# Kernel optimization log

Hardware: AMD Instinct MI355X
Metric: run time of the kernel (lower is better)

The kernel has to match this reference:

```python
import jax, jax.numpy as jnp
import numpy as np

B, T, H, E, D, K = 4, 4096, 2048, 8, 1024, 2

def setup_inputs() -> dict:
    key = jax.random.key(0)
    ks = jax.random.split(key, 7)
    x  = jax.random.normal(ks[0], (B, T, H), dtype=jnp.float32)
    Wr = jax.random.normal(ks[1], (H, E), dtype=jnp.float32) * (1.0 / np.sqrt(H))
    br = jnp.zeros((E,), dtype=jnp.float32)
    We = jax.random.normal(ks[2], (E, H, D), dtype=jnp.float32) * (1.0 / np.sqrt(H))
    be = jnp.zeros((E, D), dtype=jnp.float32)
    Wc = jax.random.normal(ks[3], (D, H), dtype=jnp.float32) * (1.0 / np.sqrt(D))
    bc = jnp.zeros((H,), dtype=jnp.float32)
    return {"x": x, "Wr": Wr, "br": br, "We": We, "be": be, "Wc": Wc, "bc": bc}

def reference(x, Wr, br, We, be, Wc, bc):
    # Router: [B,T,H] @ [H,E] -> [B,T,E]
    router_logits = jnp.einsum('bth,he->bte', x, Wr) + br
    scores = jax.nn.softmax(router_logits, axis=-1)
    # top-k over experts (sorted descending, like torch.topk)
    topk_scores, topk_idx = jax.lax.top_k(scores, K)  # [B,T,K]
    # Dense all-expert linear: [B,T,E,D]
    expert_outs = jnp.einsum('bth,ehd->bted', x, We) + be
    # Gather the chosen experts per token: [B,T,K,D]
    gather_idx = jnp.broadcast_to(topk_idx[..., None], (B, T, K, D))
    chosen = jnp.take_along_axis(expert_outs, gather_idx, axis=2)
    # Weighted sum over top-k: [B,T,D]
    weighted = jnp.sum(chosen * topk_scores[..., None], axis=2)
    # Combine: [B,T,D] @ [D,H] -> [B,T,H]
    return jnp.einsum('btd,dh->bth', weighted, Wc) + bc
```

## Files before the change

### kernel.cpp

```cpp
#include <hip/hip_runtime.h>
#include <hip/hip_bf16.h>

typedef float f32x4 __attribute__((ext_vector_type(4)));
typedef short bf16x8 __attribute__((ext_vector_type(8)));

#define M_NT 16
#define M_OFF 17
#define M_TBL 32
#define MAX_TILES 264
#define NCHUNK 1024

__device__ __forceinline__ void gload16(const void* g, void* l) {
  __builtin_amdgcn_global_load_lds(
      (const __attribute__((address_space(1))) void*)g,
      (__attribute__((address_space(3))) void*)l, 16, 0, 0);
}

__device__ __forceinline__ float bf2f(unsigned short u) {
  union { unsigned int i; float f; } v; v.i = ((unsigned int)u) << 16; return v.f;
}
__device__ __forceinline__ unsigned short f2bf(float f) {
  __hip_bfloat16 h = __float2bfloat16(f);
  return __builtin_bit_cast(unsigned short, h);
}

#define CBAR() do { asm volatile("" ::: "memory"); __builtin_amdgcn_s_barrier(); asm volatile("" ::: "memory"); } while (0)
#define VMC4() asm volatile("s_waitcnt vmcnt(4)" ::: "memory")
#define VMC0() asm volatile("s_waitcnt vmcnt(0)" ::: "memory")

__global__ __launch_bounds__(256) void prep_kernel(
    const float* __restrict__ x, const float* __restrict__ Wr,
    const float* __restrict__ br, unsigned short* __restrict__ xbf,
    float* __restrict__ scores, int* __restrict__ idx,
    int* __restrict__ blk_hist,
    const float* __restrict__ We, unsigned short* __restrict__ WeT,
    const float* __restrict__ Wc, unsigned short* __restrict__ WcT) {
  __shared__ float tile[32][33];
  __shared__ int cnt[8];
  int blk = blockIdx.x;
  int tid = threadIdx.x;
  if (blk < NCHUNK) {
    int lane = tid & 63, w = tid >> 6;
    if (tid < 8) cnt[tid] = 0;
    __syncthreads();
    int t0 = blk * 16 + w * 4;
    const float* xr = x + (size_t)t0 * 2048;
    unsigned short* xo = xbf + (size_t)t0 * 2048;
    float acc[4][8] = {};
#pragma unroll
    for (int j = 0; j < 8; ++j) {
      int h0 = j * 256 + lane * 4;
      float4 xv[4];
#pragma unroll
      for (int t = 0; t < 4; ++t) xv[t] = *(const float4*)(xr + (size_t)t * 2048 + h0);
#pragma unroll
      for (int t = 0; t < 4; ++t) {
        ushort4 p;
        p.x = f2bf(xv[t].x); p.y = f2bf(xv[t].y);
        p.z = f2bf(xv[t].z); p.w = f2bf(xv[t].w);
        *(ushort4*)(xo + (size_t)t * 2048 + h0) = p;
      }
      const float4* wp = (const float4*)(Wr + (size_t)h0 * 8);
#pragma unroll
      for (int c = 0; c < 4; ++c) {
        float4 w0 = wp[2 * c], w1 = wp[2 * c + 1];
        float xc0 = (c == 0) ? xv[0].x : (c == 1) ? xv[0].y : (c == 2) ? xv[0].z : xv[0].w;
        float xc1 = (c == 0) ? xv[1].x : (c == 1) ? xv[1].y : (c == 2) ? xv[1].z : xv[1].w;
        float xc2 = (c == 0) ? xv[2].x : (c == 1) ? xv[2].y : (c == 2) ? xv[2].z : xv[2].w;
        float xc3 = (c == 0) ? xv[3].x : (c == 1) ? xv[3].y : (c == 2) ? xv[3].z : xv[3].w;
        acc[0][0] += xc0 * w0.x; acc[0][1] += xc0 * w0.y; acc[0][2] += xc0 * w0.z; acc[0][3] += xc0 * w0.w;
        acc[0][4] += xc0 * w1.x; acc[0][5] += xc0 * w1.y; acc[0][6] += xc0 * w1.z; acc[0][7] += xc0 * w1.w;
        acc[1][0] += xc1 * w0.x; acc[1][1] += xc1 * w0.y; acc[1][2] += xc1 * w0.z; acc[1][3] += xc1 * w0.w;
        acc[1][4] += xc1 * w1.x; acc[1][5] += xc1 * w1.y; acc[1][6] += xc1 * w1.z; acc[1][7] += xc1 * w1.w;
        acc[2][0] += xc2 * w0.x; acc[2][1] += xc2 * w0.y; acc[2][2] += xc2 * w0.z; acc[2][3] += xc2 * w0.w;
        acc[2][4] += xc2 * w1.x; acc[2][5] += xc2 * w1.y; acc[2][6] += xc2 * w1.z; acc[2][7] += xc2 * w1.w;
        acc[3][0] += xc3 * w0.x; acc[3][1] += xc3 * w0.y; acc[3][2] += xc3 * w0.z; acc[3][3] += xc3 * w0.w;
        acc[3][4] += xc3 * w1.x; acc[3][5] += xc3 * w1.y; acc[3][6] += xc3 * w1.z; acc[3][7] += xc3 * w1.w;
      }
    }
#pragma unroll
    for (int t = 0; t < 4; ++t)
#pragma unroll
      for (int e = 0; e < 8; ++e)
#pragma unroll
        for (int off = 32; off > 0; off >>= 1)
          acc[t][e] += __shfl_xor(acc[t][e], off);
    if (lane < 4) {
      int t = t0 + lane;
      float l[8];
#pragma unroll
      for (int e = 0; e < 8; ++e) {
        float v = (lane == 0) ? acc[0][e] : (lane == 1) ? acc[1][e]
                : (lane == 2) ? acc[2][e] : acc[3][e];
        l[e] = v + br[e];
      }
      float mx = l[0];
#pragma unroll
      for (int e = 1; e < 8; ++e) mx = fmaxf(mx, l[e]);
      float se = 0.f;
#pragma unroll
      for (int e = 0; e < 8; ++e) se += __expf(l[e] - mx);
      float inv = 1.f / se;
      int e1 = 0; float b1 = l[0];
#pragma unroll
      for (int e = 1; e < 8; ++e) if (l[e] > b1) { b1 = l[e]; e1 = e; }
      int e2 = -1; float b2 = -1e30f;
#pragma unroll
      for (int e = 0; e < 8; ++e) if (e != e1 && l[e] > b2) { b2 = l[e]; e2 = e; }
      idx[2 * t] = e1; idx[2 * t + 1] = e2;
      scores[2 * t] = __expf(b1 - mx) * inv;
      scores[2 * t + 1] = __expf(b2 - mx) * inv;
      atomicAdd(&cnt[e1], 1);
      atomicAdd(&cnt[e2], 1);
    }
    __syncthreads();
    if (tid < 8) blk_hist[blk * 8 + tid] = cnt[tid];
  } else if (blk < NCHUNK + 16384) {
    int i2 = blk - NCHUNK;
    int b = i2 >> 11, rem = i2 & 2047;
    int r0 = (rem >> 5) * 32, c0 = (rem & 31) * 32;
    const float* src = We + (size_t)b * 2048 * 1024;
    unsigned short* dst = WeT + (size_t)b * 2048 * 1024;
    int tx = tid & 31, ty = tid >> 5;
#pragma unroll
    for (int i = 0; i < 32; i += 8)
      tile[ty + i][tx] = src[(size_t)(r0 + ty + i) * 1024 + c0 + tx];
    __syncthreads();
#pragma unroll
    for (int i = 0; i < 32; i += 8)
      dst[(size_t)(c0 + ty + i) * 2048 + r0 + tx] = f2bf(tile[tx][ty + i]);
  } else {
    int i2 = blk - NCHUNK - 16384;
    int r0 = (i2 >> 6) * 32, c0 = (i2 & 63) * 32;
    int tx = tid & 31, ty = tid >> 5;
#pragma unroll
    for (int i = 0; i < 32; i += 8)
      tile[ty + i][tx] = Wc[(size_t)(r0 + ty + i) * 2048 + c0 + tx];
    __syncthreads();
#pragma unroll
    for (int i = 0; i < 32; i += 8)
      WcT[(size_t)(c0 + ty + i) * 1024 + r0 + tx] = f2bf(tile[tx][ty + i]);
  }
}

__global__ __launch_bounds__(512) void scan_kernel(
    const int* __restrict__ blk_hist, int* __restrict__ chunk_base,
    int* __restrict__ meta, int* __restrict__ rowlist) {
  __shared__ int stot[8], soff[8], stbase[8];
  int tid = threadIdx.x, lane = tid & 63, e = tid >> 6;
  int running = 0;
  for (int g = 0; g < NCHUNK / 64; ++g) {
    int c = g * 64 + lane;
    int v = blk_hist[c * 8 + e];
    int orig = v;
#pragma unroll
    for (int off = 1; off < 64; off <<= 1) {
      int n = __shfl_up(v, off);
      if (lane >= off) v += n;
    }
    chunk_base[c * 8 + e] = running + v - orig;
    running += __shfl(v, 63);
  }
  if (lane == 0) stot[e] = running;
  __syncthreads();
  if (tid == 0) {
    int off = 0, nt = 0;
    for (int ee = 0; ee < 8; ++ee) {
      meta[M_OFF + ee] = off; soff[ee] = off;
      int tiles = (stot[ee] + 127) >> 7;
      stbase[ee] = nt;
      nt += tiles;
      off += tiles << 7;
    }
    meta[M_NT] = nt;
  }
  __syncthreads();
  int4* tbl = (int4*)(meta + M_TBL);
  for (int ee = 0; ee < 8; ++ee) {
    int c = stot[ee], tiles = (c + 127) >> 7;
    for (int t = tid; t < tiles; t += 512)
      tbl[stbase[ee] + t] = make_int4(ee, soff[ee] + t * 128, min(128, c - t * 128), 0);
    int end = tiles << 7;
    for (int i = c + tid; i < end; i += 512) rowlist[soff[ee] + i] = 0;
  }
}

__global__ void scatter_kernel(const int* __restrict__ idx,
                               const int* __restrict__ chunk_base,
                               const int* __restrict__ meta,
                               int* __restrict__ rowlist) {
  int c = blockIdx.x, lane = threadIdx.x;
  int entry = c * 32 + lane;
  int e = (lane < 32) ? idx[entry] : -1;
#pragma unroll
  for (int ee = 0; ee < 8; ++ee) {
    unsigned long long m = __ballot(e == ee);
    if (e == ee) {
      int rank = __popcll(m & ((1ull << lane) - 1));
      rowlist[meta[M_OFF + ee] + chunk_base[c * 8 + ee] + rank] = entry;
    }
  }
}


#define RD_FRAGS(BUFB) do { \
  _Pragma("unroll") for (int m_ = 0; m_ < 4; ++m_) \
    av[m_] = *(const bf16x8*)(aP + (BUFB) + m_ * 1024); \
  _Pragma("unroll") for (int n_ = 0; n_ < 4; ++n_) \
    bv[n_] = *(const bf16x8*)(bP + (BUFB) + n_ * 1024); \
} while (0)

#define MFMA16() do { \
  __builtin_amdgcn_s_setprio(1); \
  _Pragma("unroll") for (int m_ = 0; m_ < 4; ++m_) \
  _Pragma("unroll") for (int n_ = 0; n_ < 4; ++n_) \
    acc[m_][n_] = __builtin_amdgcn_mfma_f32_16x16x32_bf16(av[m_], bv[n_], acc[m_][n_], 0, 0, 0); \
  __builtin_amdgcn_s_setprio(0); \
} while (0)

#define STAGE(BUFB, KOFF) do { \
  gload16(pA0 + (KOFF), dA + (BUFB)); \
  gload16(pA1 + (KOFF), dA + (BUFB) + 4096); \
  gload16(pB0 + (KOFF), dB + (BUFB)); \
  gload16(pB1 + (KOFF), dB + (BUFB) + 4096); \
} while (0)

__global__ __launch_bounds__(256, 4) void expert_gemm(
    const unsigned short* __restrict__ xbf,
    const unsigned short* __restrict__ WeT,
    const float* __restrict__ be,
    const float* __restrict__ scores,
    const int* __restrict__ rowlist,
    const int* __restrict__ meta,
    unsigned short* __restrict__ z) {
  __shared__ char smem[32768];
  __shared__ int lrows[128];
  int nt = meta[M_NT];
  int flat = blockIdx.y * 8 + blockIdx.x;
  int work = (flat & 7) * MAX_TILES + (flat >> 3);
  int tileid = work >> 3, nb = work & 7;
  if (tileid >= nt) return;
  int4 tt = ((const int4*)(meta + M_TBL))[tileid];
  int e = tt.x, base = tt.y, valid = tt.z;
  int n0 = nb * 128;
  int tid = threadIdx.x, lane = tid & 63, w = tid >> 6;
  if (tid < 128) lrows[tid] = rowlist[base + tid];
  __syncthreads();
  int wm = w >> 1, wn = w & 1;
  int fl = lane & 15, q = lane >> 4;
  int rA = tid >> 2;
  int sl = ((tid & 3) ^ ((rA >> 1) & 3)) * 16;
  const char* pA0 = (const char*)xbf + (size_t)(lrows[rA] >> 1) * 4096 + sl;
  const char* pA1 = (const char*)xbf + (size_t)(lrows[rA + 64] >> 1) * 4096 + sl;
  const char* pB0 = (const char*)WeT + ((size_t)e * 1024 + n0 + rA) * 4096 + sl;
  const char* pB1 = (const char*)WeT + ((size_t)e * 1024 + n0 + rA + 64) * 4096 + sl;
  char* dA = smem + tid * 16;
  char* dB = smem + 8192 + tid * 16;
  int swz = ((fl >> 1) & 3) << 4;
  const char* aP = smem + (wm * 64 + fl) * 64 + ((q * 16) ^ swz);
  const char* bP = smem + 8192 + (wn * 64 + fl) * 64 + ((q * 16) ^ swz);
  STAGE(0, 0); STAGE(16384, 64);
  VMC4(); CBAR();
  f32x4 acc[4][4] = {};
  bf16x8 av[4], bv[4];
  const int NT = 64;
  for (int t2 = 0; t2 < NT; t2 += 2) {
    int koff = t2 * 64;
    RD_FRAGS(0);
    MFMA16();
    CBAR();
    if (t2 + 2 < NT) { STAGE(0, koff + 128); VMC4(); } else { VMC0(); }
    CBAR();
    RD_FRAGS(16384);
    MFMA16();
    CBAR();
    if (t2 + 3 < NT) { STAGE(16384, koff + 192); VMC4(); } else { VMC0(); }
    CBAR();
  }
  float bev[4];
#pragma unroll
  for (int nc = 0; nc < 4; ++nc)
    bev[nc] = be[e * 1024 + n0 + wn * 64 + nc * 16 + fl];
#pragma unroll
  for (int mi = 0; mi < 4; ++mi) {
    int rowbase = wm * 64 + mi * 16 + q * 4;
#pragma unroll
    for (int r = 0; r < 4; ++r) {
      int row = rowbase + r;
      if (row < valid) {
        int entry = lrows[row];
        float s = scores[entry];
        unsigned short* zr = z + (size_t)entry * 1024 + n0 + wn * 64 + fl;
#pragma unroll
        for (int nc = 0; nc < 4; ++nc)
          zr[nc * 16] = f2bf((acc[mi][nc][r] + bev[nc]) * s);
      }
    }
  }
}

__global__ __launch_bounds__(256, 4) void combine_gemm(
    const unsigned short* __restrict__ y,
    const unsigned short* __restrict__ WcT,
    const float* __restrict__ bc,
    float* __restrict__ out) {
  __shared__ char smem[32768];
  int flat = blockIdx.y * 8 + blockIdx.x;
  int work = (flat & 7) * 256 + (flat >> 3);
  int mt = work >> 4, nb = work & 15;
  int m0 = mt * 128, n0 = nb * 128;
  int tid = threadIdx.x, lane = tid & 63, w = tid >> 6;
  int wm = w >> 1, wn = w & 1;
  int fl = lane & 15, q = lane >> 4;
  int rA = tid >> 2;
  int sl = ((tid & 3) ^ ((rA >> 1) & 3)) * 16;
  const char* pA0 = (const char*)y + (size_t)(m0 + rA) * 2048 + sl;
  const char* pA1 = (const char*)y + (size_t)(m0 + rA + 64) * 2048 + sl;
  const char* pB0 = (const char*)WcT + (size_t)(n0 + rA) * 2048 + sl;
  const char* pB1 = (const char*)WcT + (size_t)(n0 + rA + 64) * 2048 + sl;
  char* dA = smem + tid * 16;
  char* dB = smem + 8192 + tid * 16;
  int swz = ((fl >> 1) & 3) << 4;
  const char* aP = smem + (wm * 64 + fl) * 64 + ((q * 16) ^ swz);
  const char* bP = smem + 8192 + (wn * 64 + fl) * 64 + ((q * 16) ^ swz);
  STAGE(0, 0); STAGE(16384, 64);
  VMC4(); CBAR();
  f32x4 acc[4][4] = {};
  bf16x8 av[4], bv[4];
  const int NT = 32;
  for (int t2 = 0; t2 < NT; t2 += 2) {
    int koff = t2 * 64;
    RD_FRAGS(0);
    MFMA16();
    CBAR();
    if (t2 + 2 < NT) { STAGE(0, koff + 128); VMC4(); } else { VMC0(); }
    CBAR();
    RD_FRAGS(16384);
    MFMA16();
    CBAR();
    if (t2 + 3 < NT) { STAGE(16384, koff + 192); VMC4(); } else { VMC0(); }
    CBAR();
  }
  float bcv[4];
#pragma unroll
  for (int nc = 0; nc < 4; ++nc)
    bcv[nc] = bc[n0 + wn * 64 + nc * 16 + fl];
#pragma unroll
  for (int mi = 0; mi < 4; ++mi) {
    int rowbase = m0 + wm * 64 + mi * 16 + q * 4;
#pragma unroll
    for (int r = 0; r < 4; ++r) {
      float* orow = out + (size_t)(rowbase + r) * 2048 + n0 + wn * 64 + fl;
#pragma unroll
      for (int nc = 0; nc < 4; ++nc)
        orow[nc * 16] = acc[mi][nc][r] + bcv[nc];
    }
  }
}

__global__ void wsum_kernel(const unsigned short* __restrict__ z,
                            unsigned short* __restrict__ y) {
  size_t i = ((size_t)blockIdx.x * 256 + threadIdx.x) * 8;
  size_t t = i >> 10, d = i & 1023;
  int4 za = *(const int4*)(z + (t * 2) * 1024 + d);
  int4 zb = *(const int4*)(z + (t * 2 + 1) * 1024 + d);
  int4 r;
  const unsigned short* pa = (const unsigned short*)&za;
  const unsigned short* pb = (const unsigned short*)&zb;
  unsigned short* pr = (unsigned short*)&r;
#pragma unroll
  for (int j = 0; j < 8; ++j) pr[j] = f2bf(bf2f(pa[j]) + bf2f(pb[j]));
  *(int4*)(y + i) = r;
}

extern "C" void kernel_launch(void* const* d_in, const int* in_sizes, int n_in,
                              void* d_out, int out_size, void* d_ws, size_t ws_size,
                              hipStream_t stream) {
  const float* x  = (const float*)d_in[0];
  const float* Wr = (const float*)d_in[1];
  const float* br = (const float*)d_in[2];
  const float* We = (const float*)d_in[3];
  const float* be = (const float*)d_in[4];
  const float* Wc = (const float*)d_in[5];
  const float* bc = (const float*)d_in[6];
  float* out = (float*)d_out;

  char* ws = (char*)d_ws;
  size_t o = 0;
  auto alloc = [&](size_t b) {
    char* p = ws + o;
    o = (o + b + 255) & ~(size_t)255;
    return p;
  };
  unsigned short* xbf = (unsigned short*)alloc(16384UL * 2048 * 2);
  unsigned short* WeT = (unsigned short*)alloc(8UL * 1024 * 2048 * 2);
  unsigned short* WcT = (unsigned short*)alloc(2048UL * 1024 * 2);
  unsigned short* z   = (unsigned short*)alloc(32768UL * 1024 * 2);
  unsigned short* yw  = (unsigned short*)alloc(16384UL * 1024 * 2);
  float* scores = (float*)alloc(32768UL * 4);
  int* idx      = (int*)alloc(32768UL * 4);
  int* rowlist  = (int*)alloc(36864UL * 4);
  int* meta     = (int*)alloc(8192);
  int* blk_hist = (int*)alloc(NCHUNK * 8 * 4);
  int* chunk_base = (int*)alloc(NCHUNK * 8 * 4);
  (void)ws_size; (void)in_sizes; (void)n_in; (void)out_size;

  hipLaunchKernelGGL(prep_kernel, dim3(NCHUNK + 16384 + 2048), dim3(256), 0, stream,
                     x, Wr, br, xbf, scores, idx, blk_hist, We, WeT, Wc, WcT);
  hipLaunchKernelGGL(scan_kernel, dim3(1), dim3(512), 0, stream, blk_hist, chunk_base, meta, rowlist);
  hipLaunchKernelGGL(scatter_kernel, dim3(NCHUNK), dim3(64), 0, stream, idx, chunk_base, meta, rowlist);
  hipLaunchKernelGGL(expert_gemm, dim3(8, MAX_TILES), dim3(256), 0, stream,
                     xbf, WeT, be, scores, rowlist, meta, z);
  hipLaunchKernelGGL(wsum_kernel, dim3(8192), dim3(256), 0, stream, z, yw);
  hipLaunchKernelGGL(combine_gemm, dim3(8, 256), dim3(256), 0, stream, yw, WcT, bc, out);
}
```

Measured before the change: 376.0 us.

## Switch expert and combine GEMMs to triple-buffered LDS pipeline with one barrier per tile

Both GEMM kernels move from a double-buffered K loop with two barriers per tile to a three-stage LDS ring. The next-next tile's loads are issued before the current tile's fragment reads and MFMAs, leaving one barrier per K step. This is meant to hide global-to-LDS latency and cut barrier stalls. The cost is 48KB of shared memory per block and launch bounds lowered from 4 to 3 blocks per CU, so occupancy drops.

```diff
diff --git a/kernel.cpp b/kernel.cpp
--- a/kernel.cpp
+++ b/kernel.cpp
@@ -225,7 +225,15 @@
   gload16(pB1 + (KOFF), dB + (BUFB) + 4096); \
 } while (0)
 
-__global__ __launch_bounds__(256, 4) void expert_gemm(
+#define KT1(BUFR, BUFS, T, NTT) do { \
+  if ((T) + 2 < (NTT)) STAGE(BUFS, ((T) + 2) * 64); \
+  RD_FRAGS(BUFR); \
+  MFMA16(); \
+  if ((T) + 2 < (NTT)) { VMC4(); } else { VMC0(); } \
+  CBAR(); \
+} while (0)
+
+__global__ __launch_bounds__(256, 3) void expert_gemm(
     const unsigned short* __restrict__ xbf,
     const unsigned short* __restrict__ WeT,
     const float* __restrict__ be,
@@ -233,7 +241,7 @@
     const int* __restrict__ rowlist,
     const int* __restrict__ meta,
     unsigned short* __restrict__ z) {
-  __shared__ char smem[32768];
+  __shared__ char smem[49152];
   __shared__ int lrows[128];
   int nt = meta[M_NT];
   int flat = blockIdx.y * 8 + blockIdx.x;
@@ -264,19 +272,12 @@
   f32x4 acc[4][4] = {};
   bf16x8 av[4], bv[4];
   const int NT = 64;
-  for (int t2 = 0; t2 < NT; t2 += 2) {
-    int koff = t2 * 64;
-    RD_FRAGS(0);
-    MFMA16();
-    CBAR();
-    if (t2 + 2 < NT) { STAGE(0, koff + 128); VMC4(); } else { VMC0(); }
-    CBAR();
-    RD_FRAGS(16384);
-    MFMA16();
-    CBAR();
-    if (t2 + 3 < NT) { STAGE(16384, koff + 192); VMC4(); } else { VMC0(); }
-    CBAR();
-  }
+  for (int t = 0; t < NT - 1; t += 3) {
+    KT1(0,     32768, t,     NT);
+    KT1(16384, 0,     t + 1, NT);
+    KT1(32768, 16384, t + 2, NT);
+  }
+  KT1(0, 32768, NT - 1, NT);
   float bev[4];
 #pragma unroll
   for (int nc = 0; nc < 4; ++nc)
@@ -299,12 +300,12 @@
   }
 }
 
-__global__ __launch_bounds__(256, 4) void combine_gemm(
+__global__ __launch_bounds__(256, 3) void combine_gemm(
     const unsigned short* __restrict__ y,
     const unsigned short* __restrict__ WcT,
     const float* __restrict__ bc,
     float* __restrict__ out) {
-  __shared__ char smem[32768];
+  __shared__ char smem[49152];
   int flat = blockIdx.y * 8 + blockIdx.x;
   int work = (flat & 7) * 256 + (flat >> 3);
   int mt = work >> 4, nb = work & 15;
@@ -328,19 +329,13 @@
   f32x4 acc[4][4] = {};
   bf16x8 av[4], bv[4];
   const int NT = 32;
-  for (int t2 = 0; t2 < NT; t2 += 2) {
-    int koff = t2 * 64;
-    RD_FRAGS(0);
-    MFMA16();
-    CBAR();
-    if (t2 + 2 < NT) { STAGE(0, koff + 128); VMC4(); } else { VMC0(); }
-    CBAR();
-    RD_FRAGS(16384);
-    MFMA16();
-    CBAR();
-    if (t2 + 3 < NT) { STAGE(16384, koff + 192); VMC4(); } else { VMC0(); }
-    CBAR();
-  }
+  for (int t = 0; t < NT - 2; t += 3) {
+    KT1(0,     32768, t,     NT);
+    KT1(16384, 0,     t + 1, NT);
+    KT1(32768, 16384, t + 2, NT);
+  }
+  KT1(0, 32768, NT - 2, NT);
+  KT1(16384, 0, NT - 1, NT);
   float bcv[4];
 #pragma unroll
   for (int nc = 0; nc < 4; ++nc)
```

Measured after the change: 378.0 us. About the same (+0.5%).
